# Kernel optimization log

Measured on AMD Instinct MI355X. Metric: run time of the kernel, lower is better.

Reference implementation:

```python
import jax, jax.numpy as jnp
import numpy as np

N_NODES = 100000
N_EDGES = 1600000
D_IN = 64
D_OUT = 64


def setup_inputs() -> dict:
    key = jax.random.key(0)
    k1, k2, k3, k4 = jax.random.split(key, 4)
    x = jax.random.normal(k1, (N_NODES, D_IN), dtype=jnp.float32)
    edge_index = jax.random.randint(k2, (2, N_EDGES), 0, N_NODES, dtype=jnp.int64)
    W = jax.random.normal(k3, (D_OUT, D_IN), dtype=jnp.float32) * (1.0 / np.sqrt(D_IN))
    b = jax.random.normal(k4, (D_OUT,), dtype=jnp.float32) * 0.01
    return {"x": x, "edge_index": edge_index, "W": W, "b": b}


def reference(x, edge_index, W, b):
    num_nodes = x.shape[0]
    row, col = edge_index[0], edge_index[1]
    # degree of each node as a destination (scatter_add of ones over row)
    deg = jax.ops.segment_sum(jnp.ones(row.shape[0], dtype=x.dtype), row,
                              num_segments=num_nodes)
    # deg^-0.5 with inf (deg==0) replaced by 0
    deg_inv_sqrt = jnp.where(deg > 0, jax.lax.rsqrt(jnp.maximum(deg, 1.0)) * jnp.where(deg > 0, 1.0, 0.0), 0.0)
    deg_inv_sqrt = jnp.where(deg > 0, deg ** -0.5, 0.0)
    # gather source features, scale by source norm, scatter-add to destinations
    weighted = x[col] * deg_inv_sqrt[col][:, None]          # [E, D_IN]
    agg = jax.ops.segment_sum(weighted, row, num_segments=num_nodes)  # [N, D_IN]
    agg = agg * deg_inv_sqrt[:, None]
    # linear + relu (torch Linear: y = agg @ W.T + b)
    return jax.nn.relu(agg @ W.T + b)
```

## Files before the change

kernel.cpp:

```cpp
#include <hip/hip_runtime.h>

#define N_NODES 100000
#define N_EDGES 1600000
#define D 64

#define FSHIFT 5
#define FNODES 32
#define NFB 3125
#define CAPF 800

#define CSHIFT 11
#define NCB 49
#define CCAP 36864
#define FPC 64
#define NCHUNKB 9

#define CHUNK 4096
#define EPT 16
#define NCHUNKA 391

#define COLBITS 17
#define COLMASK 0x1FFFF

#define FCUR_OFF   0
#define CCUR_OFF   16384
#define CPAIRS_OFF 32768
#define FPAIRS_OFF 7258112
#define Y_OFF      17258112

__device__ __forceinline__ float bf2f(unsigned short u) {
    return __uint_as_float(((unsigned)u) << 16);
}
__device__ __forceinline__ unsigned f2bf(float f) {
    unsigned bits = __float_as_uint(f);
    return (bits + 0x7FFFu + ((bits >> 16) & 1u)) >> 16;
}

__global__ void initcur_kernel(int* __restrict__ fcur, int* __restrict__ ccur) {
    int i = blockIdx.x * blockDim.x + threadIdx.x;
    if (i < NFB) fcur[i] = i * CAPF;
    if (i < NCB) ccur[i] = i * CCAP;
}

__global__ __launch_bounds__(256) void scatA_kernel(const int* __restrict__ row,
                                                    const int* __restrict__ col,
                                                    int* __restrict__ ccur,
                                                    int* __restrict__ cpairs) {
    __shared__ int lcnt[NCB];
    int t = threadIdx.x;
    int base = blockIdx.x * CHUNK;
    if (t < NCB) lcnt[t] = 0;
    __syncthreads();
    int r[EPT], c[EPT], pos[EPT];
#pragma unroll
    for (int i = 0; i < EPT; ++i) {
        int e = base + i * 256 + t;
        if (e < N_EDGES) {
            r[i] = row[e];
            c[i] = col[e];
            pos[i] = atomicAdd(&lcnt[r[i] >> CSHIFT], 1);
        } else r[i] = -1;
    }
    __syncthreads();
    if (t < NCB) {
        int cc = lcnt[t];
        if (cc) lcnt[t] = atomicAdd(&ccur[t], cc);
    }
    __syncthreads();
#pragma unroll
    for (int i = 0; i < EPT; ++i) {
        if (r[i] >= 0) {
            int cb = r[i] >> CSHIFT;
            int rl = r[i] & ((1 << CSHIFT) - 1);
            cpairs[lcnt[cb] + pos[i]] = (rl << COLBITS) | c[i];
        }
    }
}

__global__ __launch_bounds__(256) void scatB_kernel(const int* __restrict__ cpairs,
                                                    const int* __restrict__ ccur,
                                                    int* __restrict__ fcur,
                                                    int* __restrict__ fpairs) {
    __shared__ int lcnt[FPC];
    int t = threadIdx.x;
    int cb = blockIdx.x / NCHUNKB;
    int k  = blockIdx.x % NCHUNKB;
    int beg = cb * CCAP + k * CHUNK;
    int end = ccur[cb];
    if (end > beg + CHUNK) end = beg + CHUNK;
    if (t < FPC) lcnt[t] = 0;
    __syncthreads();
    int pc[EPT], pos[EPT];
#pragma unroll
    for (int i = 0; i < EPT; ++i) {
        int e = beg + i * 256 + t;
        if (e < end) {
            pc[i] = cpairs[e];
            pos[i] = atomicAdd(&lcnt[pc[i] >> (COLBITS + FSHIFT)], 1);
        } else pc[i] = -1;
    }
    __syncthreads();
    if (t < FPC) {
        int cc = lcnt[t];
        if (cc) lcnt[t] = atomicAdd(&fcur[(cb << 6) + t], cc);
    }
    __syncthreads();
#pragma unroll
    for (int i = 0; i < EPT; ++i) {
        if (pc[i] >= 0) {
            int fl = pc[i] >> (COLBITS + FSHIFT);
            int rl5 = (pc[i] >> COLBITS) & (FNODES - 1);
            fpairs[lcnt[fl] + pos[i]] = (rl5 << COLBITS) | (pc[i] & COLMASK);
        }
    }
}

__global__ __launch_bounds__(256) void xform_kernel(
        const float* __restrict__ x, const float* __restrict__ W,
        const int* __restrict__ fpairs, const int* __restrict__ fcur,
        unsigned short* __restrict__ y) {
    __shared__ __align__(16) float XT[D * 68];
    __shared__ __align__(16) float WT[D * 68];
    __shared__ int hist[64];
    __shared__ float dl[64];
    int t = threadIdx.x;
    int b = blockIdx.x;
    int nb0 = b << 6;
    for (int i = t; i < D * D; i += 256) {
        int j = i >> 6, d = i & 63;
        WT[d * 68 + j] = W[i];
    }
    if (t < 64) hist[t] = 0;
    __syncthreads();
    for (int i = t; i < 64 * D; i += 256) {
        int n = i >> 6, d = i & 63;
        int g = nb0 + n;
        XT[d * 68 + n] = (g < N_NODES) ? x[(size_t)g * D + d] : 0.0f;
    }
#pragma unroll
    for (int half = 0; half < 2; ++half) {
        int f = 2 * b + half;
        if (f < NFB) {
            int beg = f * CAPF, end = fcur[f];
            for (int k = beg + t; k < end; k += 256)
                atomicAdd(&hist[(fpairs[k] >> COLBITS) + (half << FSHIFT)], 1);
        }
    }
    __syncthreads();
    if (t < 64) dl[t] = (hist[t] > 0) ? rsqrtf((float)hist[t]) : 0.0f;
    __syncthreads();
    int tj = t & 15, tn = t >> 4;
    float4 a0 = {0,0,0,0}, a1 = {0,0,0,0}, a2 = {0,0,0,0}, a3 = {0,0,0,0};
#pragma unroll 8
    for (int d = 0; d < D; ++d) {
        float4 xv = *(const float4*)&XT[d * 68 + tn * 4];
        float4 wv = *(const float4*)&WT[d * 68 + tj * 4];
        a0.x = fmaf(xv.x, wv.x, a0.x); a0.y = fmaf(xv.x, wv.y, a0.y);
        a0.z = fmaf(xv.x, wv.z, a0.z); a0.w = fmaf(xv.x, wv.w, a0.w);
        a1.x = fmaf(xv.y, wv.x, a1.x); a1.y = fmaf(xv.y, wv.y, a1.y);
        a1.z = fmaf(xv.y, wv.z, a1.z); a1.w = fmaf(xv.y, wv.w, a1.w);
        a2.x = fmaf(xv.z, wv.x, a2.x); a2.y = fmaf(xv.z, wv.y, a2.y);
        a2.z = fmaf(xv.z, wv.z, a2.z); a2.w = fmaf(xv.z, wv.w, a2.w);
        a3.x = fmaf(xv.w, wv.x, a3.x); a3.y = fmaf(xv.w, wv.y, a3.y);
        a3.z = fmaf(xv.w, wv.z, a3.z); a3.w = fmaf(xv.w, wv.w, a3.w);
    }
    int jb = tj * 4;
#pragma unroll
    for (int s = 0; s < 4; ++s) {
        int g = nb0 + tn * 4 + s;
        if (g < N_NODES) {
            float sc = dl[tn * 4 + s];
            float4 a = (s == 0) ? a0 : (s == 1) ? a1 : (s == 2) ? a2 : a3;
            unsigned lo = f2bf(a.x * sc) | (f2bf(a.y * sc) << 16);
            unsigned hi = f2bf(a.z * sc) | (f2bf(a.w * sc) << 16);
            *(uint2*)(y + (size_t)g * D + jb) = make_uint2(lo, hi);
        }
    }
}

__global__ __launch_bounds__(256) void mega_kernel(
        const int* __restrict__ fpairs, const int* __restrict__ fcur,
        const unsigned short* __restrict__ y,
        const float* __restrict__ bias, float* __restrict__ out) {
    __shared__ int hist[FNODES];
    __shared__ int sc[FNODES];
    __shared__ int lrptr[FNODES + 1];
    __shared__ int lcur[FNODES];
    __shared__ float dl[FNODES];
    __shared__ int lds_scol[CAPF];
    int t = threadIdx.x;
    int b = blockIdx.x;
    int beg = b * CAPF, end = fcur[b];
    if (t < FNODES) hist[t] = 0;
    __syncthreads();
    for (int k = beg + t; k < end; k += 256)
        atomicAdd(&hist[fpairs[k] >> COLBITS], 1);
    __syncthreads();
    if (t < FNODES) sc[t] = hist[t];
    __syncthreads();
    for (int off = 1; off < FNODES; off <<= 1) {
        int v = (t < FNODES && t >= off) ? sc[t - off] : 0;
        __syncthreads();
        if (t < FNODES) sc[t] += v;
        __syncthreads();
    }
    if (t < FNODES) {
        lrptr[t + 1] = sc[t];
        lcur[t] = sc[t] - hist[t];
        dl[t] = (hist[t] > 0) ? rsqrtf((float)hist[t]) : 0.0f;
    }
    if (t == 0) lrptr[0] = 0;
    __syncthreads();
    for (int k = beg + t; k < end; k += 256) {
        int p = fpairs[k];
        int pos = atomicAdd(&lcur[p >> COLBITS], 1);
        lds_scol[pos] = p & COLMASK;
    }
    __syncthreads();
    int wave = t >> 6, j = t & 63;
    float bj = bias[j];
    for (int ln = wave; ln < FNODES; ln += 4) {
        int s = lrptr[ln], e2 = lrptr[ln + 1];
        float a0 = 0, a1 = 0, a2 = 0, a3 = 0, a4 = 0, a5 = 0, a6 = 0, a7 = 0;
        int k = s;
        for (; k + 7 < e2; k += 8) {
            int c0 = lds_scol[k + 0], c1 = lds_scol[k + 1];
            int c2 = lds_scol[k + 2], c3 = lds_scol[k + 3];
            int c4 = lds_scol[k + 4], c5 = lds_scol[k + 5];
            int c6 = lds_scol[k + 6], c7 = lds_scol[k + 7];
            a0 += bf2f(y[(size_t)c0 * D + j]);
            a1 += bf2f(y[(size_t)c1 * D + j]);
            a2 += bf2f(y[(size_t)c2 * D + j]);
            a3 += bf2f(y[(size_t)c3 * D + j]);
            a4 += bf2f(y[(size_t)c4 * D + j]);
            a5 += bf2f(y[(size_t)c5 * D + j]);
            a6 += bf2f(y[(size_t)c6 * D + j]);
            a7 += bf2f(y[(size_t)c7 * D + j]);
        }
        for (; k < e2; ++k) a0 += bf2f(y[(size_t)lds_scol[k] * D + j]);
        float sum = ((a0 + a1) + (a2 + a3)) + ((a4 + a5) + (a6 + a7));
        int n = (b << FSHIFT) + ln;
        out[(size_t)n * D + j] = fmaxf(fmaf(dl[ln], sum, bj), 0.0f);
    }
}

extern "C" void kernel_launch(void* const* d_in, const int* in_sizes, int n_in,
                              void* d_out, int out_size, void* d_ws, size_t ws_size,
                              hipStream_t stream) {
    const float* x    = (const float*)d_in[0];
    const int*   eidx = (const int*)d_in[1];
    const float* W    = (const float*)d_in[2];
    const float* b    = (const float*)d_in[3];
    float* out = (float*)d_out;
    char* ws = (char*)d_ws;

    const int* row = eidx;
    const int* col = eidx + N_EDGES;

    int* fcur   = (int*)(ws + FCUR_OFF);
    int* ccur   = (int*)(ws + CCUR_OFF);
    int* cpairs = (int*)(ws + CPAIRS_OFF);
    int* fpairs = (int*)(ws + FPAIRS_OFF);
    unsigned short* y = (unsigned short*)(ws + Y_OFF);

    initcur_kernel<<<(NFB + 255) / 256, 256, 0, stream>>>(fcur, ccur);
    scatA_kernel<<<NCHUNKA, 256, 0, stream>>>(row, col, ccur, cpairs);
    scatB_kernel<<<NCB * NCHUNKB, 256, 0, stream>>>(cpairs, ccur, fcur, fpairs);
    xform_kernel<<<(N_NODES + 63) / 64, 256, 0, stream>>>(x, W, fpairs, fcur, y);
    mega_kernel<<<NFB, 256, 0, stream>>>(fpairs, fcur, y, b, out);
}
```

Baseline: 189.8 us.

## Vectorize bf16 gather to 16-byte loads with 8-edge lane groups

The aggregation loop switches from one bf16 feature per lane per edge to groups of 8 lanes, each lane loading 16 bytes (8 bf16 features) of a neighbor row, so a wave processes 8 edges at once. Partial sums are combined across lane groups with xor shuffles, and the result is written with vectorized nontemporal float4 stores. The aim is to cut the number of narrow gather instructions and raise per-instruction memory throughput. In exchange it adds a shuffle reduction and more registers per lane, and leaves lanes idle when a node has few edges.

```diff
diff --git a/kernel.cpp b/kernel.cpp
--- a/kernel.cpp
+++ b/kernel.cpp
@@ -27,6 +27,8 @@
 #define CPAIRS_OFF 32768
 #define FPAIRS_OFF 7258112
 #define Y_OFF      17258112
+
+typedef float fvec4 __attribute__((ext_vector_type(4)));
 
 __device__ __forceinline__ float bf2f(unsigned short u) {
     return __uint_as_float(((unsigned)u) << 16);
@@ -217,30 +219,57 @@
         lds_scol[pos] = p & COLMASK;
     }
     __syncthreads();
-    int wave = t >> 6, j = t & 63;
-    float bj = bias[j];
+    int wave = t >> 6;
+    int lane = t & 63;
+    int g = lane >> 3;
+    int q = lane & 7;
+    float bj[8];
+    {
+        float4 b0 = *(const float4*)(bias + q * 8);
+        float4 b1 = *(const float4*)(bias + q * 8 + 4);
+        bj[0] = b0.x; bj[1] = b0.y; bj[2] = b0.z; bj[3] = b0.w;
+        bj[4] = b1.x; bj[5] = b1.y; bj[6] = b1.z; bj[7] = b1.w;
+    }
     for (int ln = wave; ln < FNODES; ln += 4) {
         int s = lrptr[ln], e2 = lrptr[ln + 1];
-        float a0 = 0, a1 = 0, a2 = 0, a3 = 0, a4 = 0, a5 = 0, a6 = 0, a7 = 0;
-        int k = s;
-        for (; k + 7 < e2; k += 8) {
-            int c0 = lds_scol[k + 0], c1 = lds_scol[k + 1];
-            int c2 = lds_scol[k + 2], c3 = lds_scol[k + 3];
-            int c4 = lds_scol[k + 4], c5 = lds_scol[k + 5];
-            int c6 = lds_scol[k + 6], c7 = lds_scol[k + 7];
-            a0 += bf2f(y[(size_t)c0 * D + j]);
-            a1 += bf2f(y[(size_t)c1 * D + j]);
-            a2 += bf2f(y[(size_t)c2 * D + j]);
-            a3 += bf2f(y[(size_t)c3 * D + j]);
-            a4 += bf2f(y[(size_t)c4 * D + j]);
-            a5 += bf2f(y[(size_t)c5 * D + j]);
-            a6 += bf2f(y[(size_t)c6 * D + j]);
-            a7 += bf2f(y[(size_t)c7 * D + j]);
-        }
-        for (; k < e2; ++k) a0 += bf2f(y[(size_t)lds_scol[k] * D + j]);
-        float sum = ((a0 + a1) + (a2 + a3)) + ((a4 + a5) + (a6 + a7));
+        float a[8];
+#pragma unroll
+        for (int i = 0; i < 8; ++i) a[i] = 0.0f;
+        for (int k = s; k < e2; k += 32) {
+#pragma unroll
+            for (int u = 0; u < 4; ++u) {
+                int e = k + u * 8 + g;
+                if (e < e2) {
+                    int c = lds_scol[e];
+                    uint4 v = *(const uint4*)(y + (size_t)c * D + q * 8);
+                    a[0] += __uint_as_float(v.x << 16);
+                    a[1] += __uint_as_float(v.x & 0xffff0000u);
+                    a[2] += __uint_as_float(v.y << 16);
+                    a[3] += __uint_as_float(v.y & 0xffff0000u);
+                    a[4] += __uint_as_float(v.z << 16);
+                    a[5] += __uint_as_float(v.z & 0xffff0000u);
+                    a[6] += __uint_as_float(v.w << 16);
+                    a[7] += __uint_as_float(v.w & 0xffff0000u);
+                }
+            }
+        }
+#pragma unroll
+        for (int m = 8; m <= 32; m <<= 1) {
+#pragma unroll
+            for (int i = 0; i < 8; ++i)
+                a[i] += __shfl_xor(a[i], m);
+        }
+        float dv = dl[ln];
         int n = (b << FSHIFT) + ln;
-        out[(size_t)n * D + j] = fmaxf(fmaf(dl[ln], sum, bj), 0.0f);
+        if (g < 2) {
+            int o = g * 4;
+            fvec4 r;
+            r.x = fmaxf(fmaf(dv, a[o + 0], bj[o + 0]), 0.0f);
+            r.y = fmaxf(fmaf(dv, a[o + 1], bj[o + 1]), 0.0f);
+            r.z = fmaxf(fmaf(dv, a[o + 2], bj[o + 2]), 0.0f);
+            r.w = fmaxf(fmaf(dv, a[o + 3], bj[o + 3]), 0.0f);
+            __builtin_nontemporal_store(r, (fvec4*)(out + (size_t)n * D + q * 8 + o));
+        }
     }
 }
 
```

After: 183.8 us. 1.03x faster.
